# Kernel optimization log

Hardware: AMD Instinct MI355X
Metric: run time of the kernel (lower is better)

## Reference

```python
import jax, jax.numpy as jnp
import numpy as np

B, S, H, F, E, K = 4, 2048, 1024, 2048, 8, 2


def setup_inputs() -> dict:
    key = jax.random.key(0)
    ks = jax.random.split(key, 5)
    scale = 0.02
    return {
        "hidden_states": jax.random.normal(ks[0], (B, S, H), dtype=jnp.float32),
        "gate_w": jax.random.normal(ks[1], (E, H), dtype=jnp.float32) * scale,
        "w1": jax.random.normal(ks[2], (E, F, H), dtype=jnp.float32) * scale,
        "w3": jax.random.normal(ks[3], (E, F, H), dtype=jnp.float32) * scale,
        "w2": jax.random.normal(ks[4], (E, H, F), dtype=jnp.float32) * scale,
    }


def reference(hidden_states, gate_w, w1, w3, w2):
    b, s, h = hidden_states.shape
    x = hidden_states.reshape(-1, h)  # [T, H]
    T = x.shape[0]
    # router
    router_logits = x @ gate_w.T  # [T, E]
    probs = jax.nn.softmax(router_logits.astype(jnp.float32), axis=-1)
    routing_weights, selected = jax.lax.top_k(probs, K)  # [T, K]
    routing_weights = routing_weights / jnp.sum(routing_weights, axis=-1, keepdims=True)
    routing_weights = routing_weights.astype(x.dtype)
    # dense per-token expert weight matrix [T, E] (zero for unselected experts)
    full_w = jnp.zeros((T, gate_w.shape[0]), dtype=x.dtype)
    full_w = full_w.at[jnp.arange(T)[:, None], selected].set(routing_weights)
    out = jnp.zeros_like(x)
    for e in range(gate_w.shape[0]):
        gated = jax.nn.silu(x @ w1[e].T) * (x @ w3[e].T)  # [T, F]
        y = gated @ w2[e].T  # [T, H]
        out = out + full_w[:, e:e + 1] * y
    return out.reshape(b, s, h), router_logits
```

## Files before the change

### kernel.cpp

```cpp
#include <hip/hip_runtime.h>

typedef unsigned short ushort_t;
typedef __attribute__((ext_vector_type(8))) short short8;
typedef __attribute__((ext_vector_type(4))) float floatx4;

#define T_TOK 8192
#define HDIM 1024
#define FDIM 2048
#define NEXP 8
#define TK_SLOTS (T_TOK * 2)
#define SORT_THREADS 1024
#define PER_THREAD (TK_SLOTS / SORT_THREADS)

__device__ __forceinline__ float b2f(unsigned short u) {
    union { unsigned int i; float f; } x; x.i = ((unsigned int)u) << 16; return x.f;
}
__device__ __forceinline__ unsigned short f2b(float f) {
    unsigned int u = __float_as_uint(f);
    u += 0x7FFF + ((u >> 16) & 1);
    return (unsigned short)(u >> 16);
}
__device__ __forceinline__ void gload16(const void* g, void* l) {
    __builtin_amdgcn_global_load_lds((const __attribute__((address_space(1))) void*)g,
                                     (__attribute__((address_space(3))) void*)l,
                                     16, 0, 0);
}

__global__ __launch_bounds__(256) void cvt_kernel(
    const float* __restrict__ src, ushort_t* __restrict__ dst, int n8)
{
    int i = blockIdx.x * 256 + threadIdx.x;
    if (i >= n8) return;
    const float4* s4 = (const float4*)src;
    float4 a = s4[2 * i], b = s4[2 * i + 1];
    short8 o;
    o[0] = (short)f2b(a.x); o[1] = (short)f2b(a.y);
    o[2] = (short)f2b(a.z); o[3] = (short)f2b(a.w);
    o[4] = (short)f2b(b.x); o[5] = (short)f2b(b.y);
    o[6] = (short)f2b(b.z); o[7] = (short)f2b(b.w);
    *(short8*)&dst[(size_t)i * 8] = o;
}

__global__ __launch_bounds__(256) void router_kernel(
    const float* __restrict__ X, const float* __restrict__ GW,
    float* __restrict__ logits_out, int* __restrict__ tk_e,
    float* __restrict__ tk_w)
{
    __shared__ __align__(16) float gw[NEXP * HDIM];
    const int tid = threadIdx.x;
#pragma unroll
    for (int c = 0; c < 8; ++c) {
        int idx = (c * 256 + tid) * 4;
        *(float4*)&gw[idx] = *(const float4*)&GW[idx];
    }
    __syncthreads();
    const int w = tid >> 6, l = tid & 63;
    const int t = blockIdx.x * 4 + w;
    float acc[NEXP];
#pragma unroll
    for (int e = 0; e < NEXP; ++e) acc[e] = 0.f;
#pragma unroll
    for (int it = 0; it < 4; ++it) {
        const int colb = it * 256 + l * 4;
        float4 xv = *(const float4*)&X[(size_t)t * HDIM + colb];
#pragma unroll
        for (int e = 0; e < NEXP; ++e) {
            float4 gv = *(const float4*)&gw[e * HDIM + colb];
            acc[e] += xv.x * gv.x + xv.y * gv.y + xv.z * gv.z + xv.w * gv.w;
        }
    }
#pragma unroll
    for (int off = 32; off >= 1; off >>= 1)
#pragma unroll
        for (int e = 0; e < NEXP; ++e) acc[e] += __shfl_xor(acc[e], off, 64);

    if (l == 0) {
        float mx = acc[0];
#pragma unroll
        for (int e = 1; e < NEXP; ++e) mx = fmaxf(mx, acc[e]);
        float p[NEXP];
#pragma unroll
        for (int e = 0; e < NEXP; ++e) p[e] = __expf(acc[e] - mx);
        int e0 = 0;
#pragma unroll
        for (int e = 1; e < NEXP; ++e) if (p[e] > p[e0]) e0 = e;
        int e1 = (e0 == 0) ? 1 : 0;
#pragma unroll
        for (int e = 0; e < NEXP; ++e) if (e != e0 && p[e] > p[e1]) e1 = e;
        float den = p[e0] + p[e1];
        tk_e[t * 2] = e0; tk_e[t * 2 + 1] = e1;
        tk_w[t * 2] = p[e0] / den; tk_w[t * 2 + 1] = p[e1] / den;
#pragma unroll
        for (int e = 0; e < NEXP; ++e) logits_out[(size_t)t * NEXP + e] = acc[e];
    }
}

__global__ __launch_bounds__(SORT_THREADS) void sort_kernel(
    const int* __restrict__ tk_e, const float* __restrict__ tk_w,
    int* __restrict__ counts, int* __restrict__ offsets,
    int* __restrict__ token_list, float* __restrict__ weight_list,
    int* __restrict__ slot_of)
{
    __shared__ int hist[NEXP][SORT_THREADS];
    __shared__ int offs[NEXP];
    const int thr = threadIdx.x;
    const int base = thr * PER_THREAD;

    int ev[PER_THREAD];
    int cnt[NEXP];
#pragma unroll
    for (int e = 0; e < NEXP; ++e) cnt[e] = 0;
#pragma unroll
    for (int i = 0; i < PER_THREAD; ++i) {
        ev[i] = tk_e[base + i];
#pragma unroll
        for (int e = 0; e < NEXP; ++e) cnt[e] += (ev[i] == e);
    }
#pragma unroll
    for (int e = 0; e < NEXP; ++e) hist[e][thr] = cnt[e];
    __syncthreads();

    for (int off = 1; off < SORT_THREADS; off <<= 1) {
        int v[NEXP];
#pragma unroll
        for (int e = 0; e < NEXP; ++e) v[e] = (thr >= off) ? hist[e][thr - off] : 0;
        __syncthreads();
#pragma unroll
        for (int e = 0; e < NEXP; ++e) hist[e][thr] += v[e];
        __syncthreads();
    }

    if (thr == 0) {
        int s = 0;
#pragma unroll
        for (int e = 0; e < NEXP; ++e) {
            int c = hist[e][SORT_THREADS - 1];
            offs[e] = s; offsets[e] = s; counts[e] = c; s += c;
        }
    }
    __syncthreads();

    int run[NEXP];
#pragma unroll
    for (int e = 0; e < NEXP; ++e) run[e] = offs[e] + hist[e][thr] - cnt[e];

#pragma unroll
    for (int i = 0; i < PER_THREAD; ++i) {
        int e = ev[i];
        int slot = 0;
#pragma unroll
        for (int ee = 0; ee < NEXP; ++ee) if (e == ee) slot = run[ee]++;
        token_list[slot] = (base + i) >> 1;
        weight_list[slot] = tk_w[base + i];
        slot_of[base + i] = slot;
    }
}

template <int MODE, int NDIM, int KDIM, bool GATHER>
__global__ __launch_bounds__(256) void moe_gemm(
    const ushort_t* __restrict__ A, const ushort_t* __restrict__ W,
    const int* __restrict__ counts, const int* __restrict__ offsets,
    const int* __restrict__ token_list, const float* __restrict__ weight_list,
    const ushort_t* C1, ushort_t* Out)
{
    const int e = blockIdx.z;
    const int ne = counts[e];
    const int m0 = blockIdx.y * 128;
    if (m0 >= ne) return;
    const int n0 = blockIdx.x * 128;
    const int aoff = offsets[e];
    const ushort_t* Bw = W + (size_t)e * NDIM * KDIM;

    __shared__ __align__(16) ushort_t As[128 * 32];
    __shared__ __align__(16) ushort_t Bs[128 * 32];

    const int tid = threadIdx.x;
    const int l = tid & 63;
    const int wv = tid >> 6;
    const int wm = wv >> 1, wn = wv & 1;
    const int quad = l >> 4, tl = l & 15;

    floatx4 acc[4][4];
#pragma unroll
    for (int i = 0; i < 4; ++i)
#pragma unroll
        for (int j = 0; j < 4; ++j)
#pragma unroll
            for (int r = 0; r < 4; ++r) acc[i][j][r] = 0.f;

    const ushort_t* agp[2];
    const ushort_t* bgp[2];
    ushort_t* alds[2];
    ushort_t* blds[2];
#pragma unroll
    for (int c = 0; c < 2; ++c) {
        int chunk = c * 256 + tid;
        int row = chunk >> 2, cc = chunk & 3;
        int rowc = m0 + row; if (rowc >= ne) rowc = ne - 1;
        size_t arow = GATHER ? (size_t)token_list[aoff + rowc] : (size_t)(aoff + rowc);
        agp[c] = A + arow * KDIM + cc * 8;
        bgp[c] = Bw + (size_t)(n0 + row) * KDIM + cc * 8;
        int base = (c * 256 + (tid & ~63)) * 8;
        alds[c] = &As[base];
        blds[c] = &Bs[base];
    }

    for (int k0 = 0; k0 < KDIM; k0 += 32) {
        gload16(agp[0] + k0, alds[0]);
        gload16(agp[1] + k0, alds[1]);
        gload16(bgp[0] + k0, blds[0]);
        gload16(bgp[1] + k0, blds[1]);
        __syncthreads();
        short8 a[4], b[4];
#pragma unroll
        for (int i = 0; i < 4; ++i)
            a[i] = *(const short8*)&As[(wm * 64 + i * 16 + tl) * 32 + quad * 8];
#pragma unroll
        for (int j = 0; j < 4; ++j)
            b[j] = *(const short8*)&Bs[(wn * 64 + j * 16 + tl) * 32 + quad * 8];
#pragma unroll
        for (int i = 0; i < 4; ++i)
#pragma unroll
            for (int j = 0; j < 4; ++j)
                acc[i][j] = __builtin_amdgcn_mfma_f32_16x16x32_bf16(a[i], b[j], acc[i][j], 0, 0, 0);
        __syncthreads();
    }

#pragma unroll
    for (int i = 0; i < 4; ++i) {
        int mrow = m0 + wm * 64 + i * 16 + quad * 4;
#pragma unroll
        for (int r = 0; r < 4; ++r) {
            int m = mrow + r;
            if (m < ne) {
                float wgt = 0.f;
                if constexpr (MODE == 2) wgt = weight_list[aoff + m];
#pragma unroll
                for (int j = 0; j < 4; ++j) {
                    int col = n0 + wn * 64 + j * 16 + tl;
                    size_t oidx = (size_t)(aoff + m) * NDIM + col;
                    float v = acc[i][j][r];
                    if constexpr (MODE == 0) {
                        float s = v / (1.f + __expf(-v));
                        Out[oidx] = f2b(s);
                    } else if constexpr (MODE == 1) {
                        float c = b2f(C1[oidx]);
                        Out[oidx] = f2b(v * c);
                    } else {
                        Out[oidx] = f2b(wgt * v);
                    }
                }
            }
        }
    }
}

__global__ __launch_bounds__(256) void combine_kernel(
    const ushort_t* __restrict__ Y, const int* __restrict__ slot_of,
    float* __restrict__ OutF)
{
    int idx = blockIdx.x * 256 + threadIdx.x;
    int t = idx >> 7;
    int h8 = (idx & 127) << 3;
    int s0 = slot_of[t * 2], s1 = slot_of[t * 2 + 1];
    short8 y0 = *(const short8*)&Y[(size_t)s0 * HDIM + h8];
    short8 y1 = *(const short8*)&Y[(size_t)s1 * HDIM + h8];
    float4 o0, o1;
    o0.x = b2f((unsigned short)y0[0]) + b2f((unsigned short)y1[0]);
    o0.y = b2f((unsigned short)y0[1]) + b2f((unsigned short)y1[1]);
    o0.z = b2f((unsigned short)y0[2]) + b2f((unsigned short)y1[2]);
    o0.w = b2f((unsigned short)y0[3]) + b2f((unsigned short)y1[3]);
    o1.x = b2f((unsigned short)y0[4]) + b2f((unsigned short)y1[4]);
    o1.y = b2f((unsigned short)y0[5]) + b2f((unsigned short)y1[5]);
    o1.z = b2f((unsigned short)y0[6]) + b2f((unsigned short)y1[6]);
    o1.w = b2f((unsigned short)y0[7]) + b2f((unsigned short)y1[7]);
    float4* dst = (float4*)&OutF[(size_t)t * HDIM + h8];
    dst[0] = o0; dst[1] = o1;
}

extern "C" void kernel_launch(void* const* d_in, const int* in_sizes, int n_in,
                              void* d_out, int out_size, void* d_ws, size_t ws_size,
                              hipStream_t stream)
{
    const float* X  = (const float*)d_in[0];
    const float* GW = (const float*)d_in[1];
    const float* W1 = (const float*)d_in[2];
    const float* W3 = (const float*)d_in[3];
    const float* W2 = (const float*)d_in[4];
    float* OUT = (float*)d_out;
    float* LOGITS = OUT + (size_t)T_TOK * HDIM;

    char* p = (char*)d_ws;
    auto take = [&](size_t b) { char* q = p; p += (b + 255) & ~(size_t)255; return q; };
    ushort_t* Xb = (ushort_t*)take((size_t)T_TOK * HDIM * 2);
    ushort_t* Wb = (ushort_t*)take((size_t)NEXP * FDIM * HDIM * 2);
    ushort_t* C1 = (ushort_t*)take((size_t)TK_SLOTS * FDIM * 2);
    ushort_t* Yb = (ushort_t*)take((size_t)TK_SLOTS * HDIM * 2);
    int*   counts      = (int*)take(NEXP * 4);
    int*   offsets     = (int*)take(NEXP * 4);
    int*   tk_e        = (int*)take(TK_SLOTS * 4);
    float* tk_w        = (float*)take(TK_SLOTS * 4);
    int*   slot_of     = (int*)take(TK_SLOTS * 4);
    int*   token_list  = (int*)take(TK_SLOTS * 4);
    float* weight_list = (float*)take(TK_SLOTS * 4);

    router_kernel<<<T_TOK / 4, 256, 0, stream>>>(X, GW, LOGITS, tk_e, tk_w);
    sort_kernel<<<1, SORT_THREADS, 0, stream>>>(tk_e, tk_w, counts, offsets,
                                                token_list, weight_list, slot_of);
    cvt_kernel<<<(T_TOK * HDIM / 8) / 256, 256, 0, stream>>>(X, Xb, T_TOK * HDIM / 8);

    cvt_kernel<<<(NEXP * FDIM * HDIM / 8) / 256, 256, 0, stream>>>(W1, Wb, NEXP * FDIM * HDIM / 8);
    moe_gemm<0, FDIM, HDIM, true ><<<dim3(FDIM / 128, T_TOK / 128, NEXP), 256, 0, stream>>>(
        Xb, Wb, counts, offsets, token_list, nullptr, nullptr, C1);

    cvt_kernel<<<(NEXP * FDIM * HDIM / 8) / 256, 256, 0, stream>>>(W3, Wb, NEXP * FDIM * HDIM / 8);
    moe_gemm<1, FDIM, HDIM, true ><<<dim3(FDIM / 128, T_TOK / 128, NEXP), 256, 0, stream>>>(
        Xb, Wb, counts, offsets, token_list, nullptr, C1, C1 );

    cvt_kernel<<<(NEXP * HDIM * FDIM / 8) / 256, 256, 0, stream>>>(W2, Wb, NEXP * HDIM * FDIM / 8);
    moe_gemm<2, HDIM, FDIM, false><<<dim3(HDIM / 128, T_TOK / 128, NEXP), 256, 0, stream>>>(
        C1 , Wb, counts, offsets, token_list, weight_list, nullptr, Yb);

    combine_kernel<<<(T_TOK * HDIM / 8) / 256, 256, 0, stream>>>(Yb, slot_of, OUT);
}
```

Baseline: 620.0 us.

## Fuse gate and up projections into one GEMM and swizzle LDS layout

Merges the W1 and W3 expert GEMMs into a single kernel that loads each gathered activation tile once and accumulates both projections, applying SiLU times the up value in the epilogue. This removes one pass over the gathered inputs and the write-then-read of the intermediate buffer. It also adds an XOR-style row-dependent column swizzle to the LDS tiles in both GEMM kernels to reduce bank conflicts on fragment reads. In exchange, the fused kernel doubles its accumulator registers and LDS use, which may lower occupancy, and it needs an extra workspace buffer for the second converted weight.

```diff
diff --git a/kernel.cpp b/kernel.cpp
--- a/kernel.cpp
+++ b/kernel.cpp
@@ -25,6 +25,8 @@
                                      (__attribute__((address_space(3))) void*)l,
                                      16, 0, 0);
 }
+__device__ __forceinline__ int swz_gcol(int row, int slot) { return ((slot - (row >> 1)) & 3) * 8; }
+__device__ __forceinline__ int swz_raddr(int row, int q)   { return row * 32 + ((q + (row >> 1)) & 3) * 8; }
 
 __global__ __launch_bounds__(256) void cvt_kernel(
     const float* __restrict__ src, ushort_t* __restrict__ dst, int n8)
@@ -156,12 +158,11 @@
     }
 }
 
-template <int MODE, int NDIM, int KDIM, bool GATHER>
-__global__ __launch_bounds__(256) void moe_gemm(
-    const ushort_t* __restrict__ A, const ushort_t* __restrict__ W,
+__global__ __launch_bounds__(256) void moe_gemm13(
+    const ushort_t* __restrict__ A, const ushort_t* __restrict__ W1,
+    const ushort_t* __restrict__ W3,
     const int* __restrict__ counts, const int* __restrict__ offsets,
-    const int* __restrict__ token_list, const float* __restrict__ weight_list,
-    const ushort_t* C1, ushort_t* Out)
+    const int* __restrict__ token_list, ushort_t* __restrict__ Out)
 {
     const int e = blockIdx.z;
     const int ne = counts[e];
@@ -169,10 +170,12 @@
     if (m0 >= ne) return;
     const int n0 = blockIdx.x * 128;
     const int aoff = offsets[e];
-    const ushort_t* Bw = W + (size_t)e * NDIM * KDIM;
+    const ushort_t* B1w = W1 + (size_t)e * FDIM * HDIM;
+    const ushort_t* B3w = W3 + (size_t)e * FDIM * HDIM;
 
     __shared__ __align__(16) ushort_t As[128 * 32];
-    __shared__ __align__(16) ushort_t Bs[128 * 32];
+    __shared__ __align__(16) ushort_t B1s[128 * 32];
+    __shared__ __align__(16) ushort_t B3s[128 * 32];
 
     const int tid = threadIdx.x;
     const int l = tid & 63;
@@ -180,6 +183,101 @@
     const int wm = wv >> 1, wn = wv & 1;
     const int quad = l >> 4, tl = l & 15;
 
+    floatx4 acc1[4][4], acc3[4][4];
+#pragma unroll
+    for (int i = 0; i < 4; ++i)
+#pragma unroll
+        for (int j = 0; j < 4; ++j)
+#pragma unroll
+            for (int r = 0; r < 4; ++r) { acc1[i][j][r] = 0.f; acc3[i][j][r] = 0.f; }
+
+    const ushort_t* agp[2]; const ushort_t* b1gp[2]; const ushort_t* b3gp[2];
+    ushort_t* alds[2]; ushort_t* b1lds[2]; ushort_t* b3lds[2];
+#pragma unroll
+    for (int c = 0; c < 2; ++c) {
+        int idx = c * 256 + tid;
+        int row = idx >> 2, slot = idx & 3;
+        int gcol = swz_gcol(row, slot);
+        int rowc = m0 + row; if (rowc >= ne) rowc = ne - 1;
+        size_t arow = (size_t)token_list[aoff + rowc];
+        agp[c]  = A + arow * HDIM + gcol;
+        b1gp[c] = B1w + (size_t)(n0 + row) * HDIM + gcol;
+        b3gp[c] = B3w + (size_t)(n0 + row) * HDIM + gcol;
+        int base = (c * 256 + (tid & ~63)) * 8;
+        alds[c] = &As[base]; b1lds[c] = &B1s[base]; b3lds[c] = &B3s[base];
+    }
+
+    for (int k0 = 0; k0 < HDIM; k0 += 32) {
+        gload16(agp[0] + k0, alds[0]);
+        gload16(agp[1] + k0, alds[1]);
+        gload16(b1gp[0] + k0, b1lds[0]);
+        gload16(b1gp[1] + k0, b1lds[1]);
+        gload16(b3gp[0] + k0, b3lds[0]);
+        gload16(b3gp[1] + k0, b3lds[1]);
+        __syncthreads();
+        short8 a[4], b1[4], b3[4];
+#pragma unroll
+        for (int i = 0; i < 4; ++i) {
+            int ar = wm * 64 + i * 16 + tl;
+            a[i] = *(const short8*)&As[swz_raddr(ar, quad)];
+        }
+#pragma unroll
+        for (int j = 0; j < 4; ++j) {
+            int br = wn * 64 + j * 16 + tl;
+            b1[j] = *(const short8*)&B1s[swz_raddr(br, quad)];
+            b3[j] = *(const short8*)&B3s[swz_raddr(br, quad)];
+        }
+#pragma unroll
+        for (int i = 0; i < 4; ++i)
+#pragma unroll
+            for (int j = 0; j < 4; ++j) {
+                acc1[i][j] = __builtin_amdgcn_mfma_f32_16x16x32_bf16(a[i], b1[j], acc1[i][j], 0, 0, 0);
+                acc3[i][j] = __builtin_amdgcn_mfma_f32_16x16x32_bf16(a[i], b3[j], acc3[i][j], 0, 0, 0);
+            }
+        __syncthreads();
+    }
+
+#pragma unroll
+    for (int i = 0; i < 4; ++i) {
+        int mrow = m0 + wm * 64 + i * 16 + quad * 4;
+#pragma unroll
+        for (int r = 0; r < 4; ++r) {
+            int m = mrow + r;
+            if (m < ne) {
+#pragma unroll
+                for (int j = 0; j < 4; ++j) {
+                    int col = n0 + wn * 64 + j * 16 + tl;
+                    float v1 = acc1[i][j][r], v3 = acc3[i][j][r];
+                    float g = (v1 / (1.f + __expf(-v1))) * v3;
+                    Out[(size_t)(aoff + m) * FDIM + col] = f2b(g);
+                }
+            }
+        }
+    }
+}
+
+__global__ __launch_bounds__(256) void moe_gemm2(
+    const ushort_t* __restrict__ A, const ushort_t* __restrict__ W,
+    const int* __restrict__ counts, const int* __restrict__ offsets,
+    const float* __restrict__ weight_list, ushort_t* __restrict__ Out)
+{
+    const int e = blockIdx.z;
+    const int ne = counts[e];
+    const int m0 = blockIdx.y * 128;
+    if (m0 >= ne) return;
+    const int n0 = blockIdx.x * 128;
+    const int aoff = offsets[e];
+    const ushort_t* Bw = W + (size_t)e * HDIM * FDIM;
+
+    __shared__ __align__(16) ushort_t As[128 * 32];
+    __shared__ __align__(16) ushort_t Bs[128 * 32];
+
+    const int tid = threadIdx.x;
+    const int l = tid & 63;
+    const int wv = tid >> 6;
+    const int wm = wv >> 1, wn = wv & 1;
+    const int quad = l >> 4, tl = l & 15;
+
     floatx4 acc[4][4];
 #pragma unroll
     for (int i = 0; i < 4; ++i)
@@ -188,24 +286,21 @@
 #pragma unroll
             for (int r = 0; r < 4; ++r) acc[i][j][r] = 0.f;
 
-    const ushort_t* agp[2];
-    const ushort_t* bgp[2];
-    ushort_t* alds[2];
-    ushort_t* blds[2];
+    const ushort_t* agp[2]; const ushort_t* bgp[2];
+    ushort_t* alds[2]; ushort_t* blds[2];
 #pragma unroll
     for (int c = 0; c < 2; ++c) {
-        int chunk = c * 256 + tid;
-        int row = chunk >> 2, cc = chunk & 3;
+        int idx = c * 256 + tid;
+        int row = idx >> 2, slot = idx & 3;
+        int gcol = swz_gcol(row, slot);
         int rowc = m0 + row; if (rowc >= ne) rowc = ne - 1;
-        size_t arow = GATHER ? (size_t)token_list[aoff + rowc] : (size_t)(aoff + rowc);
-        agp[c] = A + arow * KDIM + cc * 8;
-        bgp[c] = Bw + (size_t)(n0 + row) * KDIM + cc * 8;
+        agp[c] = A + (size_t)(aoff + rowc) * FDIM + gcol;
+        bgp[c] = Bw + (size_t)(n0 + row) * FDIM + gcol;
         int base = (c * 256 + (tid & ~63)) * 8;
-        alds[c] = &As[base];
-        blds[c] = &Bs[base];
-    }
-
-    for (int k0 = 0; k0 < KDIM; k0 += 32) {
+        alds[c] = &As[base]; blds[c] = &Bs[base];
+    }
+
+    for (int k0 = 0; k0 < FDIM; k0 += 32) {
         gload16(agp[0] + k0, alds[0]);
         gload16(agp[1] + k0, alds[1]);
         gload16(bgp[0] + k0, blds[0]);
@@ -213,11 +308,15 @@
         __syncthreads();
         short8 a[4], b[4];
 #pragma unroll
-        for (int i = 0; i < 4; ++i)
-            a[i] = *(const short8*)&As[(wm * 64 + i * 16 + tl) * 32 + quad * 8];
-#pragma unroll
-        for (int j = 0; j < 4; ++j)
-            b[j] = *(const short8*)&Bs[(wn * 64 + j * 16 + tl) * 32 + quad * 8];
+        for (int i = 0; i < 4; ++i) {
+            int ar = wm * 64 + i * 16 + tl;
+            a[i] = *(const short8*)&As[swz_raddr(ar, quad)];
+        }
+#pragma unroll
+        for (int j = 0; j < 4; ++j) {
+            int br = wn * 64 + j * 16 + tl;
+            b[j] = *(const short8*)&Bs[swz_raddr(br, quad)];
+        }
 #pragma unroll
         for (int i = 0; i < 4; ++i)
 #pragma unroll
@@ -233,22 +332,11 @@
         for (int r = 0; r < 4; ++r) {
             int m = mrow + r;
             if (m < ne) {
-                float wgt = 0.f;
-                if constexpr (MODE == 2) wgt = weight_list[aoff + m];
+                float wgt = weight_list[aoff + m];
 #pragma unroll
                 for (int j = 0; j < 4; ++j) {
                     int col = n0 + wn * 64 + j * 16 + tl;
-                    size_t oidx = (size_t)(aoff + m) * NDIM + col;
-                    float v = acc[i][j][r];
-                    if constexpr (MODE == 0) {
-                        float s = v / (1.f + __expf(-v));
-                        Out[oidx] = f2b(s);
-                    } else if constexpr (MODE == 1) {
-                        float c = b2f(C1[oidx]);
-                        Out[oidx] = f2b(v * c);
-                    } else {
-                        Out[oidx] = f2b(wgt * v);
-                    }
+                    Out[(size_t)(aoff + m) * HDIM + col] = f2b(wgt * acc[i][j][r]);
                 }
             }
         }
@@ -292,10 +380,11 @@
 
     char* p = (char*)d_ws;
     auto take = [&](size_t b) { char* q = p; p += (b + 255) & ~(size_t)255; return q; };
-    ushort_t* Xb = (ushort_t*)take((size_t)T_TOK * HDIM * 2);
-    ushort_t* Wb = (ushort_t*)take((size_t)NEXP * FDIM * HDIM * 2);
-    ushort_t* C1 = (ushort_t*)take((size_t)TK_SLOTS * FDIM * 2);
-    ushort_t* Yb = (ushort_t*)take((size_t)TK_SLOTS * HDIM * 2);
+    ushort_t* Xb  = (ushort_t*)take((size_t)T_TOK * HDIM * 2);
+    ushort_t* W1b = (ushort_t*)take((size_t)NEXP * FDIM * HDIM * 2);
+    ushort_t* W3b = (ushort_t*)take((size_t)NEXP * FDIM * HDIM * 2);
+    ushort_t* G   = (ushort_t*)take((size_t)TK_SLOTS * FDIM * 2);
+    ushort_t* Yb  = (ushort_t*)take((size_t)TK_SLOTS * HDIM * 2);
     int*   counts      = (int*)take(NEXP * 4);
     int*   offsets     = (int*)take(NEXP * 4);
     int*   tk_e        = (int*)take(TK_SLOTS * 4);
@@ -308,18 +397,15 @@
     sort_kernel<<<1, SORT_THREADS, 0, stream>>>(tk_e, tk_w, counts, offsets,
                                                 token_list, weight_list, slot_of);
     cvt_kernel<<<(T_TOK * HDIM / 8) / 256, 256, 0, stream>>>(X, Xb, T_TOK * HDIM / 8);
-
-    cvt_kernel<<<(NEXP * FDIM * HDIM / 8) / 256, 256, 0, stream>>>(W1, Wb, NEXP * FDIM * HDIM / 8);
-    moe_gemm<0, FDIM, HDIM, true ><<<dim3(FDIM / 128, T_TOK / 128, NEXP), 256, 0, stream>>>(
-        Xb, Wb, counts, offsets, token_list, nullptr, nullptr, C1);
-
-    cvt_kernel<<<(NEXP * FDIM * HDIM / 8) / 256, 256, 0, stream>>>(W3, Wb, NEXP * FDIM * HDIM / 8);
-    moe_gemm<1, FDIM, HDIM, true ><<<dim3(FDIM / 128, T_TOK / 128, NEXP), 256, 0, stream>>>(
-        Xb, Wb, counts, offsets, token_list, nullptr, C1, C1 );
-
-    cvt_kernel<<<(NEXP * HDIM * FDIM / 8) / 256, 256, 0, stream>>>(W2, Wb, NEXP * HDIM * FDIM / 8);
-    moe_gemm<2, HDIM, FDIM, false><<<dim3(HDIM / 128, T_TOK / 128, NEXP), 256, 0, stream>>>(
-        C1 , Wb, counts, offsets, token_list, weight_list, nullptr, Yb);
+    cvt_kernel<<<(NEXP * FDIM * HDIM / 8) / 256, 256, 0, stream>>>(W1, W1b, NEXP * FDIM * HDIM / 8);
+    cvt_kernel<<<(NEXP * FDIM * HDIM / 8) / 256, 256, 0, stream>>>(W3, W3b, NEXP * FDIM * HDIM / 8);
+
+    moe_gemm13<<<dim3(FDIM / 128, T_TOK / 128, NEXP), 256, 0, stream>>>(
+        Xb, W1b, W3b, counts, offsets, token_list, G);
+
+    cvt_kernel<<<(NEXP * HDIM * FDIM / 8) / 256, 256, 0, stream>>>(W2, W1b, NEXP * HDIM * FDIM / 8);
+    moe_gemm2<<<dim3(HDIM / 128, T_TOK / 128, NEXP), 256, 0, stream>>>(
+        G, W1b, counts, offsets, weight_list, Yb);
 
     combine_kernel<<<(T_TOK * HDIM / 8) / 256, 256, 0, stream>>>(Yb, slot_of, OUT);
 }
```

Result: slower. 726.6 us (+17.2%).
